# Optimization experiments

Hardware: AMD Instinct MI355X
Metric: run time of the kernel (lower is better)

The kernel has to match this reference:

```python
import jax, jax.numpy as jnp
import numpy as np

DIM = 768
HEADS = 12
HEAD_DIM = DIM // HEADS
SCALE = HEAD_DIM ** -0.5


def setup_inputs() -> dict:
    key = jax.random.key(0)
    ks = jax.random.split(key, 8)
    B, N, C = 8, 1024, DIM
    s = 0.02
    return {
        "x": jax.random.normal(ks[0], (B, N, C), jnp.float32),
        "y": jax.random.normal(ks[1], (B, N, C), jnp.float32),
        "x_qkv_w": jax.random.normal(ks[2], (3 * C, C), jnp.float32) * s,
        "y_qkv_w": jax.random.normal(ks[3], (3 * C, C), jnp.float32) * s,
        "x_proj_w": jax.random.normal(ks[4], (C, C), jnp.float32) * s,
        "x_proj_b": jnp.zeros((C,), jnp.float32),
        "y_proj_w": jax.random.normal(ks[5], (C, C), jnp.float32) * s,
        "y_proj_b": jnp.zeros((C,), jnp.float32),
    }


def _split_qkv(t, qkv_w):
    # t: [B,N,C] -> q,k,v each [B,H,N,D]
    B, N, C = t.shape
    qkv = t @ qkv_w.T                      # [B,N,3C]
    qkv = qkv.reshape(B, N, 3, HEADS, HEAD_DIM).transpose(2, 0, 3, 1, 4)
    return qkv[0], qkv[1], qkv[2]


def reference(x, y, x_qkv_w, y_qkv_w, x_proj_w, x_proj_b, y_proj_w, y_proj_b):
    B, N, C = x.shape
    x_q, x_k, x_v = _split_qkv(x, x_qkv_w)
    y_q, y_k, y_v = _split_qkv(y, y_qkv_w)

    # scores: [B,H,N,N]; dropout is identity (attn_drop=0)
    x_attn = jax.nn.softmax(jnp.einsum('bhnd,bhmd->bhnm', x_q * SCALE, x_k), axis=-1)
    y_attn = jax.nn.softmax(jnp.einsum('bhnd,bhmd->bhnm', y_q * SCALE, y_k), axis=-1)

    # swapped V aggregation: x-branch attends over y_v, y-branch over x_v
    x_out = jnp.einsum('bhnm,bhmd->bhnd', x_attn, y_v).transpose(0, 2, 1, 3).reshape(B, N, C)
    y_out = jnp.einsum('bhnm,bhmd->bhnd', y_attn, x_v).transpose(0, 2, 1, 3).reshape(B, N, C)

    x_out = x_out @ x_proj_w.T + x_proj_b
    y_out = y_out @ y_proj_w.T + y_proj_b
    return (x_out, y_out)
```

## Files before the change

kernel.cpp:

```cpp
#include <hip/hip_runtime.h>
#include <stdint.h>
#include <stddef.h>

typedef unsigned short u16;
typedef __attribute__((ext_vector_type(8))) short bf16x8;
typedef __attribute__((ext_vector_type(4))) float f32x4;
typedef __attribute__((ext_vector_type(4))) unsigned short u16x4;

#define MFMA_BF16 __builtin_amdgcn_mfma_f32_16x16x32_bf16
#define VMCNT0 asm volatile("s_waitcnt vmcnt(0)" ::: "memory")
#define BAR_FULL asm volatile("s_waitcnt vmcnt(0)\n\ts_barrier" ::: "memory")

__device__ __forceinline__ u16 f2b(float x) {
  uint32_t u = __builtin_bit_cast(uint32_t, x);
  return (u16)((u + 0x7fffu + ((u >> 16) & 1u)) >> 16);
}

__device__ __forceinline__ void async16(const void* g, void* l) {
  __builtin_amdgcn_global_load_lds((const __attribute__((address_space(1))) void*)g,
                                   (__attribute__((address_space(3))) void*)l, 16, 0, 0);
}

__global__ void cvt_all(const float* __restrict__ x, const float* __restrict__ y,
                        const float* __restrict__ xqw, const float* __restrict__ yqw,
                        const float* __restrict__ xpw, const float* __restrict__ ypw,
                        u16* __restrict__ dst) {
  long i = ((long)blockIdx.x * 256 + threadIdx.x) * 4;
  const float* src;
  long off;
  if (i < 6291456)       { src = x;   off = 0; }
  else if (i < 12582912) { src = y;   off = 6291456; }
  else if (i < 14352384) { src = xqw; off = 12582912; }
  else if (i < 16121856) { src = yqw; off = 14352384; }
  else if (i < 16711680) { src = xpw; off = 16121856; }
  else                   { src = ypw; off = 16711680; }
  float4 v = *(const float4*)(src + (i - off));
  u16x4 o = { f2b(v.x), f2b(v.y), f2b(v.z), f2b(v.w) };
  *(u16x4*)(dst + i) = o;
}

__global__ __launch_bounds__(256, 2)
void qkv_gemm(const u16* __restrict__ Xb, const u16* __restrict__ Yb,
              const u16* __restrict__ Wx, const u16* __restrict__ Wy,
              u16* __restrict__ Qx, u16* __restrict__ Kx, u16* __restrict__ Vtx,
              u16* __restrict__ Qy, u16* __restrict__ Ky, u16* __restrict__ Vty) {
  __shared__ alignas(16) u16 As[128 * 64];
  __shared__ alignas(16) u16 Bs[128 * 64];
  const int br = blockIdx.z;
  const u16* A = br ? Yb : Xb;
  const u16* W = br ? Wy : Wx;
  u16* Qd = br ? Qy : Qx;
  u16* Kd = br ? Ky : Kx;
  u16* Vd = br ? Vty : Vtx;
  const int m0 = blockIdx.x * 128;
  const int j0 = blockIdx.y * 128;
  const int tid = threadIdx.x;
  const int wave = tid >> 6, lane = tid & 63;
  const int quad = lane >> 4, l16 = lane & 15;
  const int wm = wave >> 1, wn = wave & 1;
  const int srow = wave * 32 + (lane >> 3);
  const int scol = (((lane & 7) ^ ((lane >> 3) & 7)) * 8);
  const int l7 = l16 & 7;

  f32x4 acc[4][4] = {};

  for (int k0 = 0; k0 < 768; k0 += 64) {
#pragma unroll
    for (int c = 0; c < 4; ++c) {
      async16(A + (size_t)(m0 + srow + c * 8) * 768 + k0 + scol,
              (char*)As + wave * 4096 + c * 1024);
      async16(W + (size_t)(j0 + srow + c * 8) * 768 + k0 + scol,
              (char*)Bs + wave * 4096 + c * 1024);
    }
    VMCNT0;
    __syncthreads();
#pragma unroll
    for (int kc = 0; kc < 2; ++kc) {
      bf16x8 af[4], bfr[4];
#pragma unroll
      for (int t = 0; t < 4; ++t) {
        af[t]  = *(const bf16x8*)&As[(wm * 64 + t * 16 + l16) * 64 + (((kc * 4 + quad) ^ l7) * 8)];
        bfr[t] = *(const bf16x8*)&Bs[(wn * 64 + t * 16 + l16) * 64 + (((kc * 4 + quad) ^ l7) * 8)];
      }
#pragma unroll
      for (int mt = 0; mt < 4; ++mt)
#pragma unroll
        for (int nt = 0; nt < 4; ++nt)
          acc[mt][nt] = MFMA_BF16(af[mt], bfr[nt], acc[mt][nt], 0, 0, 0);
    }
    __syncthreads();
  }

  const int s3 = j0 / 768;
#pragma unroll
  for (int mt = 0; mt < 4; ++mt) {
#pragma unroll
    for (int nt = 0; nt < 4; ++nt) {
      const int j = j0 + wn * 64 + nt * 16 + l16;
      const int jr = j - s3 * 768;
      const int h = jr >> 6, d = jr & 63;
#pragma unroll
      for (int r = 0; r < 4; ++r) {
        const int m = m0 + wm * 64 + mt * 16 + quad * 4 + r;
        const int b = m >> 10, n = m & 1023;
        const size_t bh = (size_t)(b * 12 + h);
        const float v = acc[mt][nt][r];
        if (s3 == 0)      Qd[(bh * 1024 + n) * 64 + d] = f2b(v * 0.125f);
        else if (s3 == 1) Kd[(bh * 1024 + n) * 64 + d] = f2b(v);
        else              Vd[(bh * 64 + d) * 1024 + n] = f2b(v);
      }
    }
  }
}

__global__ __launch_bounds__(256, 3)
void attn_kernel(const u16* __restrict__ Qx, const u16* __restrict__ Kx, const u16* __restrict__ Vtx,
                 const u16* __restrict__ Qy, const u16* __restrict__ Ky, const u16* __restrict__ Vty,
                 u16* __restrict__ Ox, u16* __restrict__ Oy) {
  __shared__ alignas(16) u16 Ks[2][64 * 64];
  __shared__ alignas(16) u16 Vs[2][64 * 64];
  __shared__ alignas(16) u16 Ps[128 * 72];
  const int br = blockIdx.z;
  const u16* Q = br ? Qy : Qx;
  const u16* K = br ? Ky : Kx;
  const u16* V = br ? Vtx : Vty;
  u16* O = br ? Oy : Ox;
  const int bh = blockIdx.y;
  const int q0 = blockIdx.x * 128;
  const int tid = threadIdx.x;
  const int wave = tid >> 6, lane = tid & 63;
  const int quad = lane >> 4, l16 = lane & 15;
  const int l7 = l16 & 7;
  const int r8 = (lane >> 3) & 7;
  const int sw = ((lane & 7) ^ r8) * 8;

  const u16* Qb = Q + (size_t)bh * 65536;
  const u16* Kb = K + (size_t)bh * 65536;
  const u16* Vb = V + (size_t)bh * 65536;

  bf16x8 qf[2][2];
#pragma unroll
  for (int mt = 0; mt < 2; ++mt)
#pragma unroll
    for (int kc = 0; kc < 2; ++kc)
      qf[mt][kc] = *(const bf16x8*)(Qb + (size_t)(q0 + wave * 32 + mt * 16 + l16) * 64 + kc * 32 + quad * 8);

  f32x4 oacc[2][4] = {};
  f32x4 lsum[2] = {};
  bf16x8 ones;
#pragma unroll
  for (int j = 0; j < 8; ++j) ones[j] = (short)0x3f80;

  const int krow = wave * 16 + r8;

#pragma unroll
  for (int c = 0; c < 2; ++c) {
    async16(Kb + (size_t)(krow + c * 8) * 64 + sw, (char*)Ks[0] + wave * 2048 + c * 1024);
    async16(Vb + (size_t)(krow + c * 8) * 1024 + sw, (char*)Vs[0] + wave * 2048 + c * 1024);
  }

  for (int it = 0; it < 16; ++it) {
    const int p = it & 1;
    BAR_FULL;
    if (it < 15) {
      const int kv1 = (it + 1) * 64;
#pragma unroll
      for (int c = 0; c < 2; ++c) {
        async16(Kb + (size_t)(kv1 + krow + c * 8) * 64 + sw, (char*)Ks[p ^ 1] + wave * 2048 + c * 1024);
        async16(Vb + (size_t)(krow + c * 8) * 1024 + kv1 + sw, (char*)Vs[p ^ 1] + wave * 2048 + c * 1024);
      }
    }

    f32x4 sc[2][4] = {};
#pragma unroll
    for (int kc = 0; kc < 2; ++kc) {
      bf16x8 kf[4];
#pragma unroll
      for (int nt = 0; nt < 4; ++nt)
        kf[nt] = *(const bf16x8*)&Ks[p][(nt * 16 + l16) * 64 + (((kc * 4 + quad) ^ l7) * 8)];
#pragma unroll
      for (int mt = 0; mt < 2; ++mt)
#pragma unroll
        for (int nt = 0; nt < 4; ++nt)
          sc[mt][nt] = MFMA_BF16(qf[mt][kc], kf[nt], sc[mt][nt], 0, 0, 0);
    }

#pragma unroll
    for (int mt = 0; mt < 2; ++mt) {
      const int prow = wave * 32 + mt * 16 + quad * 4;
#pragma unroll
      for (int nt = 0; nt < 4; ++nt) {
        const int pcol = nt * 16 + l16;
#pragma unroll
        for (int r = 0; r < 4; ++r)
          Ps[(prow + r) * 72 + pcol] = f2b(__expf(sc[mt][nt][r]));
      }
    }

#pragma unroll
    for (int kc = 0; kc < 2; ++kc) {
      bf16x8 pf[2], vf[4];
#pragma unroll
      for (int mt = 0; mt < 2; ++mt)
        pf[mt] = *(const bf16x8*)&Ps[(wave * 32 + mt * 16 + l16) * 72 + kc * 32 + quad * 8];
#pragma unroll
      for (int nt = 0; nt < 4; ++nt)
        vf[nt] = *(const bf16x8*)&Vs[p][(nt * 16 + l16) * 64 + (((kc * 4 + quad) ^ l7) * 8)];
#pragma unroll
      for (int mt = 0; mt < 2; ++mt) {
#pragma unroll
        for (int nt = 0; nt < 4; ++nt)
          oacc[mt][nt] = MFMA_BF16(pf[mt], vf[nt], oacc[mt][nt], 0, 0, 0);
        lsum[mt] = MFMA_BF16(pf[mt], ones, lsum[mt], 0, 0, 0);
      }
    }
  }

  const int b = bh / 12, h = bh % 12;
#pragma unroll
  for (int mt = 0; mt < 2; ++mt) {
#pragma unroll
    for (int r = 0; r < 4; ++r) {
      const float inv = 1.0f / lsum[mt][r];
      const int qrow = q0 + wave * 32 + mt * 16 + quad * 4 + r;
      const size_t ob = ((size_t)(b * 1024 + qrow)) * 768 + h * 64;
#pragma unroll
      for (int nt = 0; nt < 4; ++nt)
        O[ob + nt * 16 + l16] = f2b(oacc[mt][nt][r] * inv);
    }
  }
}

__global__ __launch_bounds__(256, 2)
void proj_gemm(const u16* __restrict__ Ox, const u16* __restrict__ Oy,
               const u16* __restrict__ Pxw, const u16* __restrict__ Pyw,
               const float* __restrict__ bx, const float* __restrict__ by,
               float* __restrict__ out) {
  __shared__ alignas(16) u16 As[128 * 64];
  __shared__ alignas(16) u16 Bs[128 * 64];
  const int br = blockIdx.z;
  const u16* A = br ? Oy : Ox;
  const u16* W = br ? Pyw : Pxw;
  const float* bias = br ? by : bx;
  float* op = out + (size_t)br * 6291456;
  const int m0 = blockIdx.x * 128;
  const int j0 = blockIdx.y * 128;
  const int tid = threadIdx.x;
  const int wave = tid >> 6, lane = tid & 63;
  const int quad = lane >> 4, l16 = lane & 15;
  const int wm = wave >> 1, wn = wave & 1;
  const int srow = wave * 32 + (lane >> 3);
  const int scol = (((lane & 7) ^ ((lane >> 3) & 7)) * 8);
  const int l7 = l16 & 7;

  f32x4 acc[4][4] = {};

  for (int k0 = 0; k0 < 768; k0 += 64) {
#pragma unroll
    for (int c = 0; c < 4; ++c) {
      async16(A + (size_t)(m0 + srow + c * 8) * 768 + k0 + scol,
              (char*)As + wave * 4096 + c * 1024);
      async16(W + (size_t)(j0 + srow + c * 8) * 768 + k0 + scol,
              (char*)Bs + wave * 4096 + c * 1024);
    }
    VMCNT0;
    __syncthreads();
#pragma unroll
    for (int kc = 0; kc < 2; ++kc) {
      bf16x8 af[4], bfr[4];
#pragma unroll
      for (int t = 0; t < 4; ++t) {
        af[t]  = *(const bf16x8*)&As[(wm * 64 + t * 16 + l16) * 64 + (((kc * 4 + quad) ^ l7) * 8)];
        bfr[t] = *(const bf16x8*)&Bs[(wn * 64 + t * 16 + l16) * 64 + (((kc * 4 + quad) ^ l7) * 8)];
      }
#pragma unroll
      for (int mt = 0; mt < 4; ++mt)
#pragma unroll
        for (int nt = 0; nt < 4; ++nt)
          acc[mt][nt] = MFMA_BF16(af[mt], bfr[nt], acc[mt][nt], 0, 0, 0);
    }
    __syncthreads();
  }

#pragma unroll
  for (int mt = 0; mt < 4; ++mt) {
#pragma unroll
    for (int nt = 0; nt < 4; ++nt) {
      const int j = j0 + wn * 64 + nt * 16 + l16;
      const float bj = bias[j];
#pragma unroll
      for (int r = 0; r < 4; ++r) {
        const int m = m0 + wm * 64 + mt * 16 + quad * 4 + r;
        op[(size_t)m * 768 + j] = acc[mt][nt][r] + bj;
      }
    }
  }
}

extern "C" void kernel_launch(void* const* d_in, const int* in_sizes, int n_in,
                              void* d_out, int out_size, void* d_ws, size_t ws_size,
                              hipStream_t stream) {
  (void)in_sizes; (void)n_in; (void)out_size; (void)ws_size;
  const float* x   = (const float*)d_in[0];
  const float* y   = (const float*)d_in[1];
  const float* xqw = (const float*)d_in[2];
  const float* yqw = (const float*)d_in[3];
  const float* xpw = (const float*)d_in[4];
  const float* xpb = (const float*)d_in[5];
  const float* ypw = (const float*)d_in[6];
  const float* ypb = (const float*)d_in[7];
  float* out = (float*)d_out;

  char* p = (char*)d_ws;
  u16* Xb  = (u16*)p; p += 12582912;
  u16* Yb  = (u16*)p; p += 12582912;
  u16* Wxb = (u16*)p; p += 3538944;
  u16* Wyb = (u16*)p; p += 3538944;
  u16* Pxb = (u16*)p; p += 1179648;
  u16* Pyb = (u16*)p; p += 1179648;
  u16* Qx  = (u16*)p; p += 12582912;
  u16* Kx  = (u16*)p; p += 12582912;
  u16* Vtx = (u16*)p; p += 12582912;
  u16* Qy  = (u16*)p; p += 12582912;
  u16* Ky  = (u16*)p; p += 12582912;
  u16* Vty = (u16*)p; p += 12582912;
  u16* Ox  = Xb;
  u16* Oy  = Yb;

  cvt_all<<<16896, 256, 0, stream>>>(x, y, xqw, yqw, xpw, ypw, Xb);

  qkv_gemm<<<dim3(64, 18, 2), 256, 0, stream>>>(Xb, Yb, Wxb, Wyb,
                                                Qx, Kx, Vtx, Qy, Ky, Vty);
  attn_kernel<<<dim3(8, 96, 2), 256, 0, stream>>>(Qx, Kx, Vtx, Qy, Ky, Vty, Ox, Oy);
  proj_gemm<<<dim3(64, 6, 2), 256, 0, stream>>>(Ox, Oy, Pxb, Pyb, xpb, ypb, out);
}
```

Baseline: 315.6 us.

## Double-buffer GEMM k-loop and stage QKV epilogue through LDS for vector stores

Both the QKV and projection GEMMs now use two LDS buffers, so the global->LDS async loads for the next k-tile are issued before the MFMAs on the current tile, with one barrier per iteration. The QKV epilogue writes bf16 results into a padded LDS tile first (transposed for V) and then issues 16-byte coalesced stores, replacing scattered 2-byte stores. This raises LDS use to 64KB per block, which may cut occupancy below the launch-bounds target of 2 blocks.

```diff
diff --git a/kernel.cpp b/kernel.cpp
--- a/kernel.cpp
+++ b/kernel.cpp
@@ -8,7 +8,6 @@
 typedef __attribute__((ext_vector_type(4))) unsigned short u16x4;
 
 #define MFMA_BF16 __builtin_amdgcn_mfma_f32_16x16x32_bf16
-#define VMCNT0 asm volatile("s_waitcnt vmcnt(0)" ::: "memory")
 #define BAR_FULL asm volatile("s_waitcnt vmcnt(0)\n\ts_barrier" ::: "memory")
 
 __device__ __forceinline__ u16 f2b(float x) {
@@ -44,8 +43,7 @@
               const u16* __restrict__ Wx, const u16* __restrict__ Wy,
               u16* __restrict__ Qx, u16* __restrict__ Kx, u16* __restrict__ Vtx,
               u16* __restrict__ Qy, u16* __restrict__ Ky, u16* __restrict__ Vty) {
-  __shared__ alignas(16) u16 As[128 * 64];
-  __shared__ alignas(16) u16 Bs[128 * 64];
+  __shared__ alignas(16) char smem[65536];
   const int br = blockIdx.z;
   const u16* A = br ? Yb : Xb;
   const u16* W = br ? Wy : Wx;
@@ -62,25 +60,32 @@
   const int scol = (((lane & 7) ^ ((lane >> 3) & 7)) * 8);
   const int l7 = l16 & 7;
 
-  f32x4 acc[4][4] = {};
-
-  for (int k0 = 0; k0 < 768; k0 += 64) {
+  auto stage = [&](int k0, int p) {
 #pragma unroll
     for (int c = 0; c < 4; ++c) {
       async16(A + (size_t)(m0 + srow + c * 8) * 768 + k0 + scol,
-              (char*)As + wave * 4096 + c * 1024);
+              smem + p * 16384 + wave * 4096 + c * 1024);
       async16(W + (size_t)(j0 + srow + c * 8) * 768 + k0 + scol,
-              (char*)Bs + wave * 4096 + c * 1024);
-    }
-    VMCNT0;
-    __syncthreads();
+              smem + 32768 + p * 16384 + wave * 4096 + c * 1024);
+    }
+  };
+
+  f32x4 acc[4][4] = {};
+  stage(0, 0);
+
+  for (int kt = 0; kt < 12; ++kt) {
+    const int p = kt & 1;
+    BAR_FULL;
+    if (kt < 11) stage((kt + 1) * 64, p ^ 1);
+    const u16* Ap = (const u16*)smem + p * 8192;
+    const u16* Bp = (const u16*)smem + 16384 + p * 8192;
 #pragma unroll
     for (int kc = 0; kc < 2; ++kc) {
       bf16x8 af[4], bfr[4];
 #pragma unroll
       for (int t = 0; t < 4; ++t) {
-        af[t]  = *(const bf16x8*)&As[(wm * 64 + t * 16 + l16) * 64 + (((kc * 4 + quad) ^ l7) * 8)];
-        bfr[t] = *(const bf16x8*)&Bs[(wn * 64 + t * 16 + l16) * 64 + (((kc * 4 + quad) ^ l7) * 8)];
+        af[t]  = *(const bf16x8*)&Ap[(wm * 64 + t * 16 + l16) * 64 + (((kc * 4 + quad) ^ l7) * 8)];
+        bfr[t] = *(const bf16x8*)&Bp[(wn * 64 + t * 16 + l16) * 64 + (((kc * 4 + quad) ^ l7) * 8)];
       }
 #pragma unroll
       for (int mt = 0; mt < 4; ++mt)
@@ -88,27 +93,60 @@
         for (int nt = 0; nt < 4; ++nt)
           acc[mt][nt] = MFMA_BF16(af[mt], bfr[nt], acc[mt][nt], 0, 0, 0);
     }
+  }
+
+  __syncthreads();
+  u16* Ts = (u16*)smem;
+  const int s3 = j0 / 768;
+
+  if (s3 == 2) {
+#pragma unroll
+    for (int mt = 0; mt < 4; ++mt)
+#pragma unroll
+      for (int nt = 0; nt < 4; ++nt) {
+        const int j = wn * 64 + nt * 16 + l16;
+        const int mb = wm * 64 + mt * 16 + quad * 4;
+        u16x4 pk = { f2b(acc[mt][nt][0]), f2b(acc[mt][nt][1]),
+                     f2b(acc[mt][nt][2]), f2b(acc[mt][nt][3]) };
+        *(u16x4*)&Ts[j * 136 + mb] = pk;
+      }
     __syncthreads();
-  }
-
-  const int s3 = j0 / 768;
-#pragma unroll
-  for (int mt = 0; mt < 4; ++mt) {
-#pragma unroll
-    for (int nt = 0; nt < 4; ++nt) {
-      const int j = j0 + wn * 64 + nt * 16 + l16;
-      const int jr = j - s3 * 768;
+#pragma unroll
+    for (int rt = 0; rt < 8; ++rt) {
+      const int j = wave * 32 + rt * 4 + (lane >> 4);
+      const int mo = (lane & 15) * 8;
+      bf16x8 v = *(const bf16x8*)&Ts[j * 136 + mo];
+      const int jr = j0 + j - 1536;
       const int h = jr >> 6, d = jr & 63;
-#pragma unroll
-      for (int r = 0; r < 4; ++r) {
-        const int m = m0 + wm * 64 + mt * 16 + quad * 4 + r;
-        const int b = m >> 10, n = m & 1023;
-        const size_t bh = (size_t)(b * 12 + h);
-        const float v = acc[mt][nt][r];
-        if (s3 == 0)      Qd[(bh * 1024 + n) * 64 + d] = f2b(v * 0.125f);
-        else if (s3 == 1) Kd[(bh * 1024 + n) * 64 + d] = f2b(v);
-        else              Vd[(bh * 64 + d) * 1024 + n] = f2b(v);
-      }
+      const int gm = m0 + mo;
+      const int b = gm >> 10, n = gm & 1023;
+      *(bf16x8*)&Vd[((size_t)(b * 12 + h) * 64 + d) * 1024 + n] = v;
+    }
+  } else {
+    const float qs = s3 ? 1.0f : 0.125f;
+#pragma unroll
+    for (int mt = 0; mt < 4; ++mt)
+#pragma unroll
+      for (int nt = 0; nt < 4; ++nt) {
+        const int j = wn * 64 + nt * 16 + l16;
+#pragma unroll
+        for (int r = 0; r < 4; ++r) {
+          const int m = wm * 64 + mt * 16 + quad * 4 + r;
+          Ts[m * 136 + j] = f2b(acc[mt][nt][r] * qs);
+        }
+      }
+    __syncthreads();
+    u16* Dd = s3 ? Kd : Qd;
+#pragma unroll
+    for (int rt = 0; rt < 8; ++rt) {
+      const int m = wave * 32 + rt * 4 + (lane >> 4);
+      const int jh = (lane >> 3) & 1, jo = (lane & 7) * 8;
+      bf16x8 v = *(const bf16x8*)&Ts[m * 136 + jh * 64 + jo];
+      const int jr = j0 + jh * 64 + jo - s3 * 768;
+      const int h = jr >> 6, d = jr & 63;
+      const int gm = m0 + m;
+      const int b = gm >> 10, n = gm & 1023;
+      *(bf16x8*)&Dd[((size_t)(b * 12 + h) * 1024 + n) * 64 + d] = v;
     }
   }
 }
@@ -236,8 +274,7 @@
                const u16* __restrict__ Pxw, const u16* __restrict__ Pyw,
                const float* __restrict__ bx, const float* __restrict__ by,
                float* __restrict__ out) {
-  __shared__ alignas(16) u16 As[128 * 64];
-  __shared__ alignas(16) u16 Bs[128 * 64];
+  __shared__ alignas(16) char smem[65536];
   const int br = blockIdx.z;
   const u16* A = br ? Oy : Ox;
   const u16* W = br ? Pyw : Pxw;
@@ -253,25 +290,32 @@
   const int scol = (((lane & 7) ^ ((lane >> 3) & 7)) * 8);
   const int l7 = l16 & 7;
 
-  f32x4 acc[4][4] = {};
-
-  for (int k0 = 0; k0 < 768; k0 += 64) {
+  auto stage = [&](int k0, int p) {
 #pragma unroll
     for (int c = 0; c < 4; ++c) {
       async16(A + (size_t)(m0 + srow + c * 8) * 768 + k0 + scol,
-              (char*)As + wave * 4096 + c * 1024);
+              smem + p * 16384 + wave * 4096 + c * 1024);
       async16(W + (size_t)(j0 + srow + c * 8) * 768 + k0 + scol,
-              (char*)Bs + wave * 4096 + c * 1024);
-    }
-    VMCNT0;
-    __syncthreads();
+              smem + 32768 + p * 16384 + wave * 4096 + c * 1024);
+    }
+  };
+
+  f32x4 acc[4][4] = {};
+  stage(0, 0);
+
+  for (int kt = 0; kt < 12; ++kt) {
+    const int p = kt & 1;
+    BAR_FULL;
+    if (kt < 11) stage((kt + 1) * 64, p ^ 1);
+    const u16* Ap = (const u16*)smem + p * 8192;
+    const u16* Bp = (const u16*)smem + 16384 + p * 8192;
 #pragma unroll
     for (int kc = 0; kc < 2; ++kc) {
       bf16x8 af[4], bfr[4];
 #pragma unroll
       for (int t = 0; t < 4; ++t) {
-        af[t]  = *(const bf16x8*)&As[(wm * 64 + t * 16 + l16) * 64 + (((kc * 4 + quad) ^ l7) * 8)];
-        bfr[t] = *(const bf16x8*)&Bs[(wn * 64 + t * 16 + l16) * 64 + (((kc * 4 + quad) ^ l7) * 8)];
+        af[t]  = *(const bf16x8*)&Ap[(wm * 64 + t * 16 + l16) * 64 + (((kc * 4 + quad) ^ l7) * 8)];
+        bfr[t] = *(const bf16x8*)&Bp[(wn * 64 + t * 16 + l16) * 64 + (((kc * 4 + quad) ^ l7) * 8)];
       }
 #pragma unroll
       for (int mt = 0; mt < 4; ++mt)
@@ -279,7 +323,6 @@
         for (int nt = 0; nt < 4; ++nt)
           acc[mt][nt] = MFMA_BF16(af[mt], bfr[nt], acc[mt][nt], 0, 0, 0);
     }
-    __syncthreads();
   }
 
 #pragma unroll
```

Result: faster. 305.3 us (-3.3%).
